# Optimization experiments

Measured on AMD Instinct MI355X. Metric: run time of the kernel, lower is better.

Reference implementation:

```python
import jax, jax.numpy as jnp
import numpy as np

EPS = 1e-5

def wn(v, g):
    # weight_norm dim=0: each output row scaled to norm g
    return v * (g / jnp.linalg.norm(v, axis=1))[:, None]

def layernorm(h):
    mu = jnp.mean(h, axis=-1, keepdims=True)
    var = jnp.mean(jnp.square(h - mu), axis=-1, keepdims=True)
    return (h - mu) / jnp.sqrt(var + EPS)

def setup_inputs() -> dict:
    key = jax.random.key(0)
    ks = jax.random.split(key, 12)
    N, G = 200000, 256
    node_dim, cond_dim, out_dim = 256, 256, 512
    H = out_dim // 2  # 256
    s = lambda d: 1.0 / np.sqrt(d)
    return {
        "x": jax.random.normal(ks[0], (N, node_dim), jnp.float32),
        "cond": jax.random.normal(ks[1], (G, cond_dim), jnp.float32),
        "batch_ids": jax.random.randint(ks[2], (N,), 0, G, jnp.int32),
        # FiLM cond projection: Linear(cond_dim, 2H) weight-normed, with bias
        "v_cond": jax.random.normal(ks[3], (2 * H, cond_dim), jnp.float32) * s(cond_dim),
        "g_cond": jnp.ones((2 * H,), jnp.float32),
        "b_cond": jnp.zeros((2 * H,), jnp.float32),
        # FiLM main linear: Linear(node_dim, H) weight-normed, no bias
        "v1": jax.random.normal(ks[4], (H, node_dim), jnp.float32) * s(node_dim),
        "g1": jnp.ones((H,), jnp.float32),
        # head MLP: Linear(H,H)+ReLU+Linear(H,out_dim), both weight-normed, with bias
        "v2": jax.random.normal(ks[5], (H, H), jnp.float32) * s(H),
        "g2": jnp.ones((H,), jnp.float32),
        "b2": jnp.zeros((H,), jnp.float32),
        "v3": jax.random.normal(ks[6], (out_dim, H), jnp.float32) * s(H),
        "g3": jnp.ones((out_dim,), jnp.float32),
        "b3": jnp.zeros((out_dim,), jnp.float32),
    }

def reference(x, cond, batch_ids, v_cond, g_cond, b_cond, v1, g1, v2, g2, b2, v3, g3, b3):
    H = v1.shape[0]
    # per-graph FiLM params
    gb = cond @ wn(v_cond, g_cond).T + b_cond          # [G, 2H]
    gamma = gb[:, :H] + 1.0                            # [G, H]
    beta = gb[:, H:]                                   # [G, H]
    # node path: linear (no bias) + layernorm (no affine)
    h = layernorm(x @ wn(v1, g1).T)                    # [N, H]
    # gather per-graph FiLM to nodes, modulate, relu
    h = jax.nn.relu(h * gamma[batch_ids] + beta[batch_ids])
    # head MLP
    h = jax.nn.relu(h @ wn(v2, g2).T + b2)             # [N, H]
    logits = h @ wn(v3, g3).T + b3                     # [N, out_dim]
    return logits
```

## Files before the change

kernel.cpp:

```cpp
#include <hip/hip_runtime.h>

typedef __bf16 bf16x8 __attribute__((ext_vector_type(8)));
typedef float f32x16 __attribute__((ext_vector_type(16)));

#define K_DIM 256

__global__ void wn_kernel(const float* __restrict__ v, const float* __restrict__ gv,
                          __bf16* __restrict__ dstb, float* __restrict__ dstf) {
  const int r = blockIdx.x;
  const int l = threadIdx.x;
  const float* vr = v + (size_t)r * K_DIM;
  float4 p = *reinterpret_cast<const float4*>(vr + l * 4);
  float ss = p.x * p.x + p.y * p.y + p.z * p.z + p.w * p.w;
#pragma unroll
  for (int m = 1; m <= 32; m <<= 1) ss += __shfl_xor(ss, m, 64);
  const float sc = gv[r] * rsqrtf(ss);
  const float a0 = p.x * sc, a1 = p.y * sc, a2 = p.z * sc, a3 = p.w * sc;
  if (dstf != nullptr) {
    float4 o; o.x = a0; o.y = a1; o.z = a2; o.w = a3;
    *reinterpret_cast<float4*>(dstf + (size_t)r * K_DIM + l * 4) = o;
  }
  if (dstb != nullptr) {
    const int rows = gridDim.x;
    __bf16* d = dstb + ((size_t)(l >> 1) * rows + r) * 8 + (l & 1) * 4;
    d[0] = (__bf16)a0; d[1] = (__bf16)a1; d[2] = (__bf16)a2; d[3] = (__bf16)a3;
  }
}

__global__ void gb_kernel(const float* __restrict__ cond, const float* __restrict__ wncf,
                          const float* __restrict__ bc, float* __restrict__ gbuf) {
  const int gidx = blockIdx.x;
  const int t = threadIdx.x;
  __shared__ float c[256];
  c[t] = cond[(size_t)gidx * 256 + t];
  __syncthreads();
#pragma unroll
  for (int h = 0; h < 2; ++h) {
    const int o = (h << 8) + t;
    const float* wr = wncf + (size_t)o * 256;
    float s = 0.0f;
#pragma unroll 8
    for (int k = 0; k < 256; k += 4) {
      const float4 w4 = *reinterpret_cast<const float4*>(wr + k);
      s += c[k] * w4.x + c[k + 1] * w4.y + c[k + 2] * w4.z + c[k + 3] * w4.w;
    }
    gbuf[(size_t)gidx * 512 + o] = s + bc[o] + (h == 0 ? 1.0f : 0.0f);
  }
}

__global__ __launch_bounds__(128, 2) void fused_kernel(
    const float* __restrict__ x, const int* __restrict__ bids,
    const __bf16* __restrict__ W1t, const __bf16* __restrict__ W2t,
    const __bf16* __restrict__ W3t, const float* __restrict__ gbuf,
    const float* __restrict__ b2, const float* __restrict__ b3,
    float* __restrict__ out, const int n) {
  __shared__ __bf16 Abuf[32 * 64 * 8];
  __shared__ __bf16 Wbuf[4 * 256 * 8];

  const int t = threadIdx.x;
  const int lane = t & 63;
  const int wave = t >> 6;
  const int nlo = lane & 31;
  const int g = lane >> 5;
  const int mbase = wave << 5;
  const int R = blockIdx.x << 6;

  f32x16 zero;
#pragma unroll
  for (int e = 0; e < 16; ++e) zero[e] = 0.0f;

  f32x16 acc[8];

  auto stage_w = [&](const __bf16* wsrc, int kt, int outr, int outbase) {
#pragma unroll
    for (int it = 0; it < 8; ++it) {
      const int cid = (((wave << 3) + it) << 6) + lane;
      const int kc = cid >> 8;
      const int outl = cid & 255;
      const __bf16* gp = wsrc + ((size_t)((kt * 4 + kc) * outr + outbase + outl) << 3);
      __builtin_amdgcn_global_load_lds(
          (__attribute__((address_space(1))) void*)gp,
          (__attribute__((address_space(3))) void*)(&Wbuf[((wave << 3) + it) << 9]),
          16, 0, 0);
    }
  };

#pragma unroll
  for (int nt = 0; nt < 8; ++nt) acc[nt] = zero;
  {
    int row = R + mbase + nlo;
    if (row >= n) row = n - 1;
    const float* xrow = x + (size_t)row * K_DIM;
    for (int kt = 0; kt < 8; ++kt) {
      __syncthreads();
      stage_w(W1t, kt, 256, 0);
      __syncthreads();
#pragma unroll
      for (int ks = 0; ks < 2; ++ks) {
        const int k0 = kt * 32 + ks * 16 + g * 8;
        const float4 p = *reinterpret_cast<const float4*>(xrow + k0);
        const float4 q = *reinterpret_cast<const float4*>(xrow + k0 + 4);
        bf16x8 a;
        a[0] = (__bf16)p.x; a[1] = (__bf16)p.y; a[2] = (__bf16)p.z; a[3] = (__bf16)p.w;
        a[4] = (__bf16)q.x; a[5] = (__bf16)q.y; a[6] = (__bf16)q.z; a[7] = (__bf16)q.w;
#pragma unroll
        for (int nt = 0; nt < 8; ++nt) {
          const bf16x8 b = *reinterpret_cast<const bf16x8*>(
              &Wbuf[((((ks << 1) + g) << 8) + (nt << 5) + nlo) << 3]);
          acc[nt] = __builtin_amdgcn_mfma_f32_32x32x16_bf16(a, b, acc[nt], 0, 0, 0);
        }
      }
    }
  }

  {
    float mu[16], rs[16];
#pragma unroll
    for (int reg = 0; reg < 16; ++reg) {
      float s = 0.0f, q = 0.0f;
#pragma unroll
      for (int nt = 0; nt < 8; ++nt) {
        const float v = acc[nt][reg];
        s += v; q += v * v;
      }
#pragma unroll
      for (int m = 1; m <= 16; m <<= 1) {
        s += __shfl_xor(s, m, 64);
        q += __shfl_xor(q, m, 64);
      }
      const float mean = s * (1.0f / 256.0f);
      const float var = q * (1.0f / 256.0f) - mean * mean;
      mu[reg] = mean;
      rs[reg] = rsqrtf(var + 1e-5f);
    }
#pragma unroll
    for (int reg = 0; reg < 16; ++reg) {
      const int rl = (reg & 3) + ((reg >> 2) << 3) + (g << 2);
      int rglob = R + mbase + rl;
      if (rglob >= n) rglob = n - 1;
      const int bid = bids[rglob];
      const float* grow = gbuf + ((size_t)bid << 9);
#pragma unroll
      for (int nt = 0; nt < 8; ++nt) {
        const int col = (nt << 5) + nlo;
        float v = (acc[nt][reg] - mu[reg]) * rs[reg];
        v = v * grow[col] + grow[256 + col];
        v = v > 0.0f ? v : 0.0f;
        Abuf[((((col >> 3) << 6) + mbase + rl) << 3) + (col & 7)] = (__bf16)v;
      }
    }
  }

#pragma unroll
  for (int nt = 0; nt < 8; ++nt) acc[nt] = zero;
  for (int kt = 0; kt < 8; ++kt) {
    __syncthreads();
    stage_w(W2t, kt, 256, 0);
    __syncthreads();
#pragma unroll
    for (int ks = 0; ks < 2; ++ks) {
      const int kc = kt * 4 + ks * 2 + g;
      const bf16x8 a = *reinterpret_cast<const bf16x8*>(
          &Abuf[((kc << 6) + mbase + nlo) << 3]);
#pragma unroll
      for (int nt = 0; nt < 8; ++nt) {
        const bf16x8 b = *reinterpret_cast<const bf16x8*>(
            &Wbuf[((((ks << 1) + g) << 8) + (nt << 5) + nlo) << 3]);
        acc[nt] = __builtin_amdgcn_mfma_f32_32x32x16_bf16(a, b, acc[nt], 0, 0, 0);
      }
    }
  }
  {
    float b2v[8];
#pragma unroll
    for (int nt = 0; nt < 8; ++nt) b2v[nt] = b2[(nt << 5) + nlo];
#pragma unroll
    for (int reg = 0; reg < 16; ++reg) {
      const int rl = (reg & 3) + ((reg >> 2) << 3) + (g << 2);
#pragma unroll
      for (int nt = 0; nt < 8; ++nt) {
        const int col = (nt << 5) + nlo;
        float v = acc[nt][reg] + b2v[nt];
        v = v > 0.0f ? v : 0.0f;
        Abuf[((((col >> 3) << 6) + mbase + rl) << 3) + (col & 7)] = (__bf16)v;
      }
    }
  }

  for (int half = 0; half < 2; ++half) {
#pragma unroll
    for (int nt = 0; nt < 8; ++nt) acc[nt] = zero;
    for (int kt = 0; kt < 8; ++kt) {
      __syncthreads();
      stage_w(W3t, kt, 512, half << 8);
      __syncthreads();
#pragma unroll
      for (int ks = 0; ks < 2; ++ks) {
        const int kc = kt * 4 + ks * 2 + g;
        const bf16x8 a = *reinterpret_cast<const bf16x8*>(
            &Abuf[((kc << 6) + mbase + nlo) << 3]);
#pragma unroll
        for (int nt = 0; nt < 8; ++nt) {
          const bf16x8 b = *reinterpret_cast<const bf16x8*>(
              &Wbuf[((((ks << 1) + g) << 8) + (nt << 5) + nlo) << 3]);
          acc[nt] = __builtin_amdgcn_mfma_f32_32x32x16_bf16(a, b, acc[nt], 0, 0, 0);
        }
      }
    }
    float b3v[8];
#pragma unroll
    for (int nt = 0; nt < 8; ++nt) b3v[nt] = b3[(half << 8) + (nt << 5) + nlo];
#pragma unroll
    for (int reg = 0; reg < 16; ++reg) {
      const int rl = (reg & 3) + ((reg >> 2) << 3) + (g << 2);
      const int rglob = R + mbase + rl;
      if (rglob < n) {
        float* orow = out + (size_t)rglob * 512 + (half << 8);
#pragma unroll
        for (int nt = 0; nt < 8; ++nt) orow[(nt << 5) + nlo] = acc[nt][reg] + b3v[nt];
      }
    }
  }
}

extern "C" void kernel_launch(void* const* d_in, const int* in_sizes, int n_in,
                              void* d_out, int out_size, void* d_ws, size_t ws_size,
                              hipStream_t stream) {
  const float* x      = (const float*)d_in[0];
  const float* cond   = (const float*)d_in[1];
  const int*   bids   = (const int*)d_in[2];
  const float* v_cond = (const float*)d_in[3];
  const float* g_cond = (const float*)d_in[4];
  const float* b_cond = (const float*)d_in[5];
  const float* v1     = (const float*)d_in[6];
  const float* g1     = (const float*)d_in[7];
  const float* v2     = (const float*)d_in[8];
  const float* g2     = (const float*)d_in[9];
  const float* b2     = (const float*)d_in[10];
  const float* v3     = (const float*)d_in[11];
  const float* g3     = (const float*)d_in[12];
  const float* b3     = (const float*)d_in[13];
  float* out = (float*)d_out;
  const int n = in_sizes[0] / K_DIM;

  char* ws = (char*)d_ws;
  __bf16* W1t = (__bf16*)ws;
  __bf16* W2t = W1t + 65536;
  __bf16* W3t = W2t + 65536;
  float* wncf = (float*)(W3t + 131072);
  float* gbuf = wncf + 131072;

  wn_kernel<<<256, 64, 0, stream>>>(v1, g1, W1t, nullptr);
  wn_kernel<<<256, 64, 0, stream>>>(v2, g2, W2t, nullptr);
  wn_kernel<<<512, 64, 0, stream>>>(v3, g3, W3t, nullptr);
  wn_kernel<<<512, 64, 0, stream>>>(v_cond, g_cond, nullptr, wncf);
  gb_kernel<<<256, 256, 0, stream>>>(cond, wncf, b_cond, gbuf);

  const int nb = (n + 63) / 64;
  fused_kernel<<<nb, 128, 0, stream>>>(x, bids, W1t, W2t, W3t, gbuf, b2, b3, out, n);
}
```

Before: 722.2 us.

## Split fused MLP across 8 waves with double-buffered weight staging

Measured after the change: 785.7 us. 1.09x slower.

```diff
diff --git a/kernel.cpp b/kernel.cpp
--- a/kernel.cpp
+++ b/kernel.cpp
@@ -48,78 +48,134 @@
   }
 }
 
-__global__ __launch_bounds__(128, 2) void fused_kernel(
+__global__ __launch_bounds__(512, 4) void fused_kernel(
     const float* __restrict__ x, const int* __restrict__ bids,
     const __bf16* __restrict__ W1t, const __bf16* __restrict__ W2t,
     const __bf16* __restrict__ W3t, const float* __restrict__ gbuf,
     const float* __restrict__ b2, const float* __restrict__ b3,
     float* __restrict__ out, const int n) {
   __shared__ __bf16 Abuf[32 * 64 * 8];
-  __shared__ __bf16 Wbuf[4 * 256 * 8];
+  __shared__ __bf16 Wbuf[2][4 * 256 * 8];
 
   const int t = threadIdx.x;
   const int lane = t & 63;
-  const int wave = t >> 6;
+  const int w = t >> 6;
+  const int wrow = w & 1;
+  const int wcol = w >> 1;
   const int nlo = lane & 31;
   const int g = lane >> 5;
-  const int mbase = wave << 5;
+  const int mbase = wrow << 5;
+  const int colbase = wcol << 6;
   const int R = blockIdx.x << 6;
 
   f32x16 zero;
 #pragma unroll
   for (int e = 0; e < 16; ++e) zero[e] = 0.0f;
 
-  f32x16 acc[8];
-
-  auto stage_w = [&](const __bf16* wsrc, int kt, int outr, int outbase) {
-#pragma unroll
-    for (int it = 0; it < 8; ++it) {
-      const int cid = (((wave << 3) + it) << 6) + lane;
+  f32x16 acc[2];
+
+  auto stage_w = [&](int buf, const __bf16* wsrc, int kt, int outr, int outbase) {
+#pragma unroll
+    for (int it = 0; it < 2; ++it) {
+      const int cid = (it << 9) + t;
       const int kc = cid >> 8;
       const int outl = cid & 255;
       const __bf16* gp = wsrc + ((size_t)((kt * 4 + kc) * outr + outbase + outl) << 3);
       __builtin_amdgcn_global_load_lds(
           (__attribute__((address_space(1))) void*)gp,
-          (__attribute__((address_space(3))) void*)(&Wbuf[((wave << 3) + it) << 9]),
+          (__attribute__((address_space(3))) void*)(&Wbuf[buf][((it << 9) + (w << 6)) << 3]),
           16, 0, 0);
     }
   };
 
-#pragma unroll
-  for (int nt = 0; nt < 8; ++nt) acc[nt] = zero;
+  auto pass_lds = [&](const __bf16* wsrc, int outr, int outbase) {
+    stage_w(0, wsrc, 0, outr, outbase);
+    __syncthreads();
+#pragma unroll
+    for (int kt = 0; kt < 8; ++kt) {
+      const int cur = kt & 1;
+      if (kt < 7) stage_w(cur ^ 1, wsrc, kt + 1, outr, outbase);
+#pragma unroll
+      for (int ks = 0; ks < 2; ++ks) {
+        const int kcf = kt * 4 + ks * 2 + g;
+        const bf16x8 a = *reinterpret_cast<const bf16x8*>(
+            &Abuf[((kcf << 6) + mbase + nlo) << 3]);
+#pragma unroll
+        for (int nt = 0; nt < 2; ++nt) {
+          const bf16x8 b = *reinterpret_cast<const bf16x8*>(
+              &Wbuf[cur][((((ks << 1) + g) << 8) + colbase + (nt << 5) + nlo) << 3]);
+          acc[nt] = __builtin_amdgcn_mfma_f32_32x32x16_bf16(a, b, acc[nt], 0, 0, 0);
+        }
+      }
+      __syncthreads();
+    }
+  };
+
+#pragma unroll
+  for (int nt = 0; nt < 2; ++nt) acc[nt] = zero;
   {
     int row = R + mbase + nlo;
     if (row >= n) row = n - 1;
     const float* xrow = x + (size_t)row * K_DIM;
+
+    stage_w(0, W1t, 0, 256, 0);
+    float4 xf[2][4];
+#pragma unroll
+    for (int i = 0; i < 2; ++i) {
+      xf[0][2 * i]     = *reinterpret_cast<const float4*>(xrow + (i << 4) + (g << 3));
+      xf[0][2 * i + 1] = *reinterpret_cast<const float4*>(xrow + (i << 4) + (g << 3) + 4);
+    }
+    __syncthreads();
+
+#pragma unroll
     for (int kt = 0; kt < 8; ++kt) {
+      const int cur = kt & 1;
+      if (kt < 7) stage_w(cur ^ 1, W1t, kt + 1, 256, 0);
+      bf16x8 a[2];
+#pragma unroll
+      for (int ks = 0; ks < 2; ++ks) {
+        const float4 p = xf[cur][2 * ks], q = xf[cur][2 * ks + 1];
+        a[ks][0] = (__bf16)p.x; a[ks][1] = (__bf16)p.y;
+        a[ks][2] = (__bf16)p.z; a[ks][3] = (__bf16)p.w;
+        a[ks][4] = (__bf16)q.x; a[ks][5] = (__bf16)q.y;
+        a[ks][6] = (__bf16)q.z; a[ks][7] = (__bf16)q.w;
+      }
+      if (kt < 7) {
+        const float* xb = xrow + ((kt + 1) << 5) + (g << 3);
+#pragma unroll
+        for (int i = 0; i < 2; ++i) {
+          xf[cur ^ 1][2 * i]     = *reinterpret_cast<const float4*>(xb + (i << 4));
+          xf[cur ^ 1][2 * i + 1] = *reinterpret_cast<const float4*>(xb + (i << 4) + 4);
+        }
+      }
+#pragma unroll
+      for (int ks = 0; ks < 2; ++ks) {
+#pragma unroll
+        for (int nt = 0; nt < 2; ++nt) {
+          const bf16x8 b = *reinterpret_cast<const bf16x8*>(
+              &Wbuf[cur][((((ks << 1) + g) << 8) + colbase + (nt << 5) + nlo) << 3]);
+          acc[nt] = __builtin_amdgcn_mfma_f32_32x32x16_bf16(a[ks], b, acc[nt], 0, 0, 0);
+        }
+      }
       __syncthreads();
-      stage_w(W1t, kt, 256, 0);
-      __syncthreads();
-#pragma unroll
-      for (int ks = 0; ks < 2; ++ks) {
-        const int k0 = kt * 32 + ks * 16 + g * 8;
-        const float4 p = *reinterpret_cast<const float4*>(xrow + k0);
-        const float4 q = *reinterpret_cast<const float4*>(xrow + k0 + 4);
-        bf16x8 a;
-        a[0] = (__bf16)p.x; a[1] = (__bf16)p.y; a[2] = (__bf16)p.z; a[3] = (__bf16)p.w;
-        a[4] = (__bf16)q.x; a[5] = (__bf16)q.y; a[6] = (__bf16)q.z; a[7] = (__bf16)q.w;
-#pragma unroll
-        for (int nt = 0; nt < 8; ++nt) {
-          const bf16x8 b = *reinterpret_cast<const bf16x8*>(
-              &Wbuf[((((ks << 1) + g) << 8) + (nt << 5) + nlo) << 3]);
-          acc[nt] = __builtin_amdgcn_mfma_f32_32x32x16_bf16(a, b, acc[nt], 0, 0, 0);
-        }
-      }
     }
   }
 
   {
-    float mu[16], rs[16];
+    float* red = reinterpret_cast<float*>(&Wbuf[0][0]);
+    int bidv[16];
+#pragma unroll
+    for (int reg = 0; reg < 16; ++reg) {
+      const int rl = (reg & 3) + ((reg >> 2) << 3) + (g << 2);
+      int rglob = R + mbase + rl;
+      if (rglob >= n) rglob = n - 1;
+      bidv[reg] = bids[rglob];
+    }
 #pragma unroll
     for (int reg = 0; reg < 16; ++reg) {
       float s = 0.0f, q = 0.0f;
 #pragma unroll
-      for (int nt = 0; nt < 8; ++nt) {
+      for (int nt = 0; nt < 2; ++nt) {
         const float v = acc[nt][reg];
         s += v; q += v * v;
       }
@@ -128,88 +184,68 @@
         s += __shfl_xor(s, m, 64);
         q += __shfl_xor(q, m, 64);
       }
+      if (nlo == 0) {
+        const int rl = (reg & 3) + ((reg >> 2) << 3) + (g << 2);
+        const int row = mbase + rl;
+        red[(row << 3) + (wcol << 1)] = s;
+        red[(row << 3) + (wcol << 1) + 1] = q;
+      }
+    }
+    __syncthreads();
+#pragma unroll
+    for (int reg = 0; reg < 16; ++reg) {
+      const int rl = (reg & 3) + ((reg >> 2) << 3) + (g << 2);
+      const int row = mbase + rl;
+      const float4 f1 = *reinterpret_cast<const float4*>(&red[row << 3]);
+      const float4 f2 = *reinterpret_cast<const float4*>(&red[(row << 3) + 4]);
+      const float s = f1.x + f1.z + f2.x + f2.z;
+      const float q = f1.y + f1.w + f2.y + f2.w;
       const float mean = s * (1.0f / 256.0f);
       const float var = q * (1.0f / 256.0f) - mean * mean;
-      mu[reg] = mean;
-      rs[reg] = rsqrtf(var + 1e-5f);
-    }
-#pragma unroll
-    for (int reg = 0; reg < 16; ++reg) {
-      const int rl = (reg & 3) + ((reg >> 2) << 3) + (g << 2);
-      int rglob = R + mbase + rl;
-      if (rglob >= n) rglob = n - 1;
-      const int bid = bids[rglob];
-      const float* grow = gbuf + ((size_t)bid << 9);
-#pragma unroll
-      for (int nt = 0; nt < 8; ++nt) {
-        const int col = (nt << 5) + nlo;
-        float v = (acc[nt][reg] - mu[reg]) * rs[reg];
+      const float rs = rsqrtf(var + 1e-5f);
+      const float* grow = gbuf + ((size_t)bidv[reg] << 9);
+#pragma unroll
+      for (int nt = 0; nt < 2; ++nt) {
+        const int col = colbase + (nt << 5) + nlo;
+        float v = (acc[nt][reg] - mean) * rs;
         v = v * grow[col] + grow[256 + col];
         v = v > 0.0f ? v : 0.0f;
-        Abuf[((((col >> 3) << 6) + mbase + rl) << 3) + (col & 7)] = (__bf16)v;
-      }
-    }
-  }
-
-#pragma unroll
-  for (int nt = 0; nt < 8; ++nt) acc[nt] = zero;
-  for (int kt = 0; kt < 8; ++kt) {
-    __syncthreads();
-    stage_w(W2t, kt, 256, 0);
-    __syncthreads();
-#pragma unroll
-    for (int ks = 0; ks < 2; ++ks) {
-      const int kc = kt * 4 + ks * 2 + g;
-      const bf16x8 a = *reinterpret_cast<const bf16x8*>(
-          &Abuf[((kc << 6) + mbase + nlo) << 3]);
-#pragma unroll
-      for (int nt = 0; nt < 8; ++nt) {
-        const bf16x8 b = *reinterpret_cast<const bf16x8*>(
-            &Wbuf[((((ks << 1) + g) << 8) + (nt << 5) + nlo) << 3]);
-        acc[nt] = __builtin_amdgcn_mfma_f32_32x32x16_bf16(a, b, acc[nt], 0, 0, 0);
-      }
-    }
-  }
+        Abuf[((((col >> 3) << 6) + row) << 3) + (col & 7)] = (__bf16)v;
+      }
+    }
+  }
+  __syncthreads();
+
+#pragma unroll
+  for (int nt = 0; nt < 2; ++nt) acc[nt] = zero;
+  pass_lds(W2t, 256, 0);
   {
-    float b2v[8];
-#pragma unroll
-    for (int nt = 0; nt < 8; ++nt) b2v[nt] = b2[(nt << 5) + nlo];
-#pragma unroll
-    for (int reg = 0; reg < 16; ++reg) {
-      const int rl = (reg & 3) + ((reg >> 2) << 3) + (g << 2);
-#pragma unroll
-      for (int nt = 0; nt < 8; ++nt) {
-        const int col = (nt << 5) + nlo;
+    float b2v[2];
+#pragma unroll
+    for (int nt = 0; nt < 2; ++nt) b2v[nt] = b2[colbase + (nt << 5) + nlo];
+#pragma unroll
+    for (int reg = 0; reg < 16; ++reg) {
+      const int rl = (reg & 3) + ((reg >> 2) << 3) + (g << 2);
+      const int row = mbase + rl;
+#pragma unroll
+      for (int nt = 0; nt < 2; ++nt) {
+        const int col = colbase + (nt << 5) + nlo;
         float v = acc[nt][reg] + b2v[nt];
         v = v > 0.0f ? v : 0.0f;
-        Abuf[((((col >> 3) << 6) + mbase + rl) << 3) + (col & 7)] = (__bf16)v;
-      }
-    }
-  }
-
+        Abuf[((((col >> 3) << 6) + row) << 3) + (col & 7)] = (__bf16)v;
+      }
+    }
+  }
+  __syncthreads();
+
+#pragma unroll
   for (int half = 0; half < 2; ++half) {
 #pragma unroll
-    for (int nt = 0; nt < 8; ++nt) acc[nt] = zero;
-    for (int kt = 0; kt < 8; ++kt) {
-      __syncthreads();
-      stage_w(W3t, kt, 512, half << 8);
-      __syncthreads();
-#pragma unroll
-      for (int ks = 0; ks < 2; ++ks) {
-        const int kc = kt * 4 + ks * 2 + g;
-        const bf16x8 a = *reinterpret_cast<const bf16x8*>(
-            &Abuf[((kc << 6) + mbase + nlo) << 3]);
-#pragma unroll
-        for (int nt = 0; nt < 8; ++nt) {
-          const bf16x8 b = *reinterpret_cast<const bf16x8*>(
-              &Wbuf[((((ks << 1) + g) << 8) + (nt << 5) + nlo) << 3]);
-          acc[nt] = __builtin_amdgcn_mfma_f32_32x32x16_bf16(a, b, acc[nt], 0, 0, 0);
-        }
-      }
-    }
-    float b3v[8];
-#pragma unroll
-    for (int nt = 0; nt < 8; ++nt) b3v[nt] = b3[(half << 8) + (nt << 5) + nlo];
+    for (int nt = 0; nt < 2; ++nt) acc[nt] = zero;
+    pass_lds(W3t, 512, half << 8);
+    float b3v[2];
+#pragma unroll
+    for (int nt = 0; nt < 2; ++nt) b3v[nt] = b3[(half << 8) + colbase + (nt << 5) + nlo];
 #pragma unroll
     for (int reg = 0; reg < 16; ++reg) {
       const int rl = (reg & 3) + ((reg >> 2) << 3) + (g << 2);
@@ -217,7 +253,8 @@
       if (rglob < n) {
         float* orow = out + (size_t)rglob * 512 + (half << 8);
 #pragma unroll
-        for (int nt = 0; nt < 8; ++nt) orow[(nt << 5) + nlo] = acc[nt][reg] + b3v[nt];
+        for (int nt = 0; nt < 2; ++nt)
+          orow[colbase + (nt << 5) + nlo] = acc[nt][reg] + b3v[nt];
       }
     }
   }
@@ -257,5 +294,5 @@
   gb_kernel<<<256, 256, 0, stream>>>(cond, wncf, b_cond, gbuf);
 
   const int nb = (n + 63) / 64;
-  fused_kernel<<<nb, 128, 0, stream>>>(x, bids, W1t, W2t, W3t, gbuf, b2, b3, out, n);
-}
+  fused_kernel<<<nb, 512, 0, stream>>>(x, bids, W1t, W2t, W3t, gbuf, b2, b3, out, n);
+}
```

## Stage full weight matrices in LDS, split columns across 4 waves, prefetch next stage

Applied to the files above, without the earlier changes.

Measured after the change: 840.0 us. 1.16x slower.

```diff
diff --git a/kernel.cpp b/kernel.cpp
--- a/kernel.cpp
+++ b/kernel.cpp
@@ -21,8 +21,8 @@
     *reinterpret_cast<float4*>(dstf + (size_t)r * K_DIM + l * 4) = o;
   }
   if (dstb != nullptr) {
-    const int rows = gridDim.x;
-    __bf16* d = dstb + ((size_t)(l >> 1) * rows + r) * 8 + (l & 1) * 4;
+    __bf16* d = dstb + ((size_t)(r >> 8) << 16) +
+                ((size_t)((l >> 1) << 8) + (r & 255)) * 8 + (l & 1) * 4;
     d[0] = (__bf16)a0; d[1] = (__bf16)a1; d[2] = (__bf16)a2; d[3] = (__bf16)a3;
   }
 }
@@ -48,78 +48,92 @@
   }
 }
 
-__global__ __launch_bounds__(128, 2) void fused_kernel(
+__global__ __launch_bounds__(256, 1) void fused_kernel(
     const float* __restrict__ x, const int* __restrict__ bids,
     const __bf16* __restrict__ W1t, const __bf16* __restrict__ W2t,
     const __bf16* __restrict__ W3t, const float* __restrict__ gbuf,
     const float* __restrict__ b2, const float* __restrict__ b3,
     float* __restrict__ out, const int n) {
+  __shared__ __bf16 Wbuf[32 * 256 * 8];
   __shared__ __bf16 Abuf[32 * 64 * 8];
-  __shared__ __bf16 Wbuf[4 * 256 * 8];
 
   const int t = threadIdx.x;
   const int lane = t & 63;
-  const int wave = t >> 6;
+  const int w = t >> 6;
+  const int rowg = w & 1;
+  const int colg = w >> 1;
   const int nlo = lane & 31;
   const int g = lane >> 5;
-  const int mbase = wave << 5;
+  const int rowbase = rowg << 5;
+  const int colbase = colg << 7;
   const int R = blockIdx.x << 6;
 
-  f32x16 zero;
-#pragma unroll
-  for (int e = 0; e < 16; ++e) zero[e] = 0.0f;
-
-  f32x16 acc[8];
-
-  auto stage_w = [&](const __bf16* wsrc, int kt, int outr, int outbase) {
-#pragma unroll
-    for (int it = 0; it < 8; ++it) {
-      const int cid = (((wave << 3) + it) << 6) + lane;
-      const int kc = cid >> 8;
-      const int outl = cid & 255;
-      const __bf16* gp = wsrc + ((size_t)((kt * 4 + kc) * outr + outbase + outl) << 3);
+  float* red = reinterpret_cast<float*>(&Wbuf[65024]);
+
+  auto aidx = [](int kc, int row) { return ((kc << 6) + (row ^ (kc & 7))) << 3; };
+
+  auto stage = [&](const __bf16* src, int U) {
+    for (int u = w; u < U; u += 4) {
       __builtin_amdgcn_global_load_lds(
-          (__attribute__((address_space(1))) void*)gp,
-          (__attribute__((address_space(3))) void*)(&Wbuf[((wave << 3) + it) << 9]),
-          16, 0, 0);
+          (__attribute__((address_space(1))) void*)(src + ((size_t)u << 9) + (lane << 3)),
+          (__attribute__((address_space(3))) void*)(&Wbuf[u << 9]), 16, 0, 0);
     }
   };
 
-#pragma unroll
-  for (int nt = 0; nt < 8; ++nt) acc[nt] = zero;
+  f32x16 acc[4];
+  auto zero_acc = [&]() {
+#pragma unroll
+    for (int nt = 0; nt < 4; ++nt)
+#pragma unroll
+      for (int e = 0; e < 16; ++e) acc[nt][e] = 0.0f;
+  };
+
+  stage(W1t, 128);
+
+  int row = R + rowbase + nlo;
+  if (row >= n) row = n - 1;
+  const float* xrow = x + (size_t)row * K_DIM;
+  float4 xp[32];
+#pragma unroll
+  for (int i = 0; i < 16; ++i) {
+    const int kc = (i << 1) + g;
+    xp[2 * i]     = *reinterpret_cast<const float4*>(xrow + (kc << 3));
+    xp[2 * i + 1] = *reinterpret_cast<const float4*>(xrow + (kc << 3) + 4);
+  }
+  int bidv[16];
+#pragma unroll
+  for (int reg = 0; reg < 16; ++reg) {
+    const int rl = (reg & 3) + ((reg >> 2) << 3) + (g << 2);
+    int rg = R + rowbase + rl;
+    if (rg >= n) rg = n - 1;
+    bidv[reg] = bids[rg];
+  }
+  __syncthreads();
+
+  zero_acc();
+#pragma unroll
+  for (int ks = 0; ks < 16; ++ks) {
+    const int kc = (ks << 1) + g;
+    const float4 p = xp[2 * ks], q = xp[2 * ks + 1];
+    bf16x8 a;
+    a[0] = (__bf16)p.x; a[1] = (__bf16)p.y; a[2] = (__bf16)p.z; a[3] = (__bf16)p.w;
+    a[4] = (__bf16)q.x; a[5] = (__bf16)q.y; a[6] = (__bf16)q.z; a[7] = (__bf16)q.w;
+#pragma unroll
+    for (int nt = 0; nt < 4; ++nt) {
+      const bf16x8 b = *reinterpret_cast<const bf16x8*>(
+          &Wbuf[((kc << 8) + colbase + (nt << 5) + nlo) << 3]);
+      acc[nt] = __builtin_amdgcn_mfma_f32_32x32x16_bf16(a, b, acc[nt], 0, 0, 0);
+    }
+  }
+  __syncthreads();
+  stage(W2t, 127);
+
   {
-    int row = R + mbase + nlo;
-    if (row >= n) row = n - 1;
-    const float* xrow = x + (size_t)row * K_DIM;
-    for (int kt = 0; kt < 8; ++kt) {
-      __syncthreads();
-      stage_w(W1t, kt, 256, 0);
-      __syncthreads();
-#pragma unroll
-      for (int ks = 0; ks < 2; ++ks) {
-        const int k0 = kt * 32 + ks * 16 + g * 8;
-        const float4 p = *reinterpret_cast<const float4*>(xrow + k0);
-        const float4 q = *reinterpret_cast<const float4*>(xrow + k0 + 4);
-        bf16x8 a;
-        a[0] = (__bf16)p.x; a[1] = (__bf16)p.y; a[2] = (__bf16)p.z; a[3] = (__bf16)p.w;
-        a[4] = (__bf16)q.x; a[5] = (__bf16)q.y; a[6] = (__bf16)q.z; a[7] = (__bf16)q.w;
-#pragma unroll
-        for (int nt = 0; nt < 8; ++nt) {
-          const bf16x8 b = *reinterpret_cast<const bf16x8*>(
-              &Wbuf[((((ks << 1) + g) << 8) + (nt << 5) + nlo) << 3]);
-          acc[nt] = __builtin_amdgcn_mfma_f32_32x32x16_bf16(a, b, acc[nt], 0, 0, 0);
-        }
-      }
-    }
-  }
-
-  {
-    float mu[16], rs[16];
 #pragma unroll
     for (int reg = 0; reg < 16; ++reg) {
       float s = 0.0f, q = 0.0f;
 #pragma unroll
-      for (int nt = 0; nt < 8; ++nt) {
+      for (int nt = 0; nt < 4; ++nt) {
         const float v = acc[nt][reg];
         s += v; q += v * v;
       }
@@ -128,96 +142,132 @@
         s += __shfl_xor(s, m, 64);
         q += __shfl_xor(q, m, 64);
       }
+      if (nlo == 0) {
+        const int rl = (reg & 3) + ((reg >> 2) << 3) + (g << 2);
+        const int rowi = rowbase + rl;
+        float2 sq; sq.x = s; sq.y = q;
+        *reinterpret_cast<float2*>(&red[(rowi << 2) + (colg << 1)]) = sq;
+      }
+    }
+    __syncthreads();
+#pragma unroll
+    for (int reg = 0; reg < 16; ++reg) {
+      const int rl = (reg & 3) + ((reg >> 2) << 3) + (g << 2);
+      const int rowi = rowbase + rl;
+      const float4 r4 = *reinterpret_cast<const float4*>(&red[rowi << 2]);
+      const float s = r4.x + r4.z, q = r4.y + r4.w;
       const float mean = s * (1.0f / 256.0f);
       const float var = q * (1.0f / 256.0f) - mean * mean;
-      mu[reg] = mean;
-      rs[reg] = rsqrtf(var + 1e-5f);
-    }
-#pragma unroll
-    for (int reg = 0; reg < 16; ++reg) {
-      const int rl = (reg & 3) + ((reg >> 2) << 3) + (g << 2);
-      int rglob = R + mbase + rl;
-      if (rglob >= n) rglob = n - 1;
-      const int bid = bids[rglob];
-      const float* grow = gbuf + ((size_t)bid << 9);
-#pragma unroll
-      for (int nt = 0; nt < 8; ++nt) {
-        const int col = (nt << 5) + nlo;
-        float v = (acc[nt][reg] - mu[reg]) * rs[reg];
+      const float rsv = rsqrtf(var + 1e-5f);
+      const float* grow = gbuf + ((size_t)bidv[reg] << 9);
+#pragma unroll
+      for (int nt = 0; nt < 4; ++nt) {
+        const int col = colbase + (nt << 5) + nlo;
+        float v = (acc[nt][reg] - mean) * rsv;
         v = v * grow[col] + grow[256 + col];
         v = v > 0.0f ? v : 0.0f;
-        Abuf[((((col >> 3) << 6) + mbase + rl) << 3) + (col & 7)] = (__bf16)v;
-      }
-    }
-  }
-
-#pragma unroll
-  for (int nt = 0; nt < 8; ++nt) acc[nt] = zero;
-  for (int kt = 0; kt < 8; ++kt) {
-    __syncthreads();
-    stage_w(W2t, kt, 256, 0);
-    __syncthreads();
-#pragma unroll
-    for (int ks = 0; ks < 2; ++ks) {
-      const int kc = kt * 4 + ks * 2 + g;
-      const bf16x8 a = *reinterpret_cast<const bf16x8*>(
-          &Abuf[((kc << 6) + mbase + nlo) << 3]);
-#pragma unroll
-      for (int nt = 0; nt < 8; ++nt) {
-        const bf16x8 b = *reinterpret_cast<const bf16x8*>(
-            &Wbuf[((((ks << 1) + g) << 8) + (nt << 5) + nlo) << 3]);
-        acc[nt] = __builtin_amdgcn_mfma_f32_32x32x16_bf16(a, b, acc[nt], 0, 0, 0);
-      }
-    }
-  }
+        Abuf[aidx(col >> 3, rowi) + (col & 7)] = (__bf16)v;
+      }
+    }
+  }
+  __syncthreads();
+  if (w == 3) {
+    __builtin_amdgcn_global_load_lds(
+        (__attribute__((address_space(1))) void*)(W2t + ((size_t)127 << 9) + (lane << 3)),
+        (__attribute__((address_space(3))) void*)(&Wbuf[127 << 9]), 16, 0, 0);
+  }
+  __syncthreads();
+
+  zero_acc();
+#pragma unroll
+  for (int ks = 0; ks < 16; ++ks) {
+    const int kc = (ks << 1) + g;
+    const bf16x8 a = *reinterpret_cast<const bf16x8*>(&Abuf[aidx(kc, rowbase + nlo)]);
+#pragma unroll
+    for (int nt = 0; nt < 4; ++nt) {
+      const bf16x8 b = *reinterpret_cast<const bf16x8*>(
+          &Wbuf[((kc << 8) + colbase + (nt << 5) + nlo) << 3]);
+      acc[nt] = __builtin_amdgcn_mfma_f32_32x32x16_bf16(a, b, acc[nt], 0, 0, 0);
+    }
+  }
+  __syncthreads();
+  stage(W3t, 128);
   {
-    float b2v[8];
-#pragma unroll
-    for (int nt = 0; nt < 8; ++nt) b2v[nt] = b2[(nt << 5) + nlo];
+    float b2v[4];
+#pragma unroll
+    for (int nt = 0; nt < 4; ++nt) b2v[nt] = b2[colbase + (nt << 5) + nlo];
 #pragma unroll
     for (int reg = 0; reg < 16; ++reg) {
       const int rl = (reg & 3) + ((reg >> 2) << 3) + (g << 2);
-#pragma unroll
-      for (int nt = 0; nt < 8; ++nt) {
-        const int col = (nt << 5) + nlo;
+      const int rowi = rowbase + rl;
+#pragma unroll
+      for (int nt = 0; nt < 4; ++nt) {
+        const int col = colbase + (nt << 5) + nlo;
         float v = acc[nt][reg] + b2v[nt];
         v = v > 0.0f ? v : 0.0f;
-        Abuf[((((col >> 3) << 6) + mbase + rl) << 3) + (col & 7)] = (__bf16)v;
-      }
-    }
-  }
-
-  for (int half = 0; half < 2; ++half) {
-#pragma unroll
-    for (int nt = 0; nt < 8; ++nt) acc[nt] = zero;
-    for (int kt = 0; kt < 8; ++kt) {
-      __syncthreads();
-      stage_w(W3t, kt, 512, half << 8);
-      __syncthreads();
-#pragma unroll
-      for (int ks = 0; ks < 2; ++ks) {
-        const int kc = kt * 4 + ks * 2 + g;
-        const bf16x8 a = *reinterpret_cast<const bf16x8*>(
-            &Abuf[((kc << 6) + mbase + nlo) << 3]);
-#pragma unroll
-        for (int nt = 0; nt < 8; ++nt) {
-          const bf16x8 b = *reinterpret_cast<const bf16x8*>(
-              &Wbuf[((((ks << 1) + g) << 8) + (nt << 5) + nlo) << 3]);
-          acc[nt] = __builtin_amdgcn_mfma_f32_32x32x16_bf16(a, b, acc[nt], 0, 0, 0);
-        }
-      }
-    }
-    float b3v[8];
-#pragma unroll
-    for (int nt = 0; nt < 8; ++nt) b3v[nt] = b3[(half << 8) + (nt << 5) + nlo];
+        Abuf[aidx(col >> 3, rowi) + (col & 7)] = (__bf16)v;
+      }
+    }
+  }
+  __syncthreads();
+
+  zero_acc();
+#pragma unroll
+  for (int ks = 0; ks < 16; ++ks) {
+    const int kc = (ks << 1) + g;
+    const bf16x8 a = *reinterpret_cast<const bf16x8*>(&Abuf[aidx(kc, rowbase + nlo)]);
+#pragma unroll
+    for (int nt = 0; nt < 4; ++nt) {
+      const bf16x8 b = *reinterpret_cast<const bf16x8*>(
+          &Wbuf[((kc << 8) + colbase + (nt << 5) + nlo) << 3]);
+      acc[nt] = __builtin_amdgcn_mfma_f32_32x32x16_bf16(a, b, acc[nt], 0, 0, 0);
+    }
+  }
+  __syncthreads();
+  stage(W3t + 65536, 128);
+  {
+    float b3v[4];
+#pragma unroll
+    for (int nt = 0; nt < 4; ++nt) b3v[nt] = b3[colbase + (nt << 5) + nlo];
 #pragma unroll
     for (int reg = 0; reg < 16; ++reg) {
       const int rl = (reg & 3) + ((reg >> 2) << 3) + (g << 2);
-      const int rglob = R + mbase + rl;
+      const int rglob = R + rowbase + rl;
       if (rglob < n) {
-        float* orow = out + (size_t)rglob * 512 + (half << 8);
-#pragma unroll
-        for (int nt = 0; nt < 8; ++nt) orow[(nt << 5) + nlo] = acc[nt][reg] + b3v[nt];
+        float* orow = out + (size_t)rglob * 512;
+#pragma unroll
+        for (int nt = 0; nt < 4; ++nt)
+          orow[colbase + (nt << 5) + nlo] = acc[nt][reg] + b3v[nt];
+      }
+    }
+  }
+  __syncthreads();
+
+  zero_acc();
+#pragma unroll
+  for (int ks = 0; ks < 16; ++ks) {
+    const int kc = (ks << 1) + g;
+    const bf16x8 a = *reinterpret_cast<const bf16x8*>(&Abuf[aidx(kc, rowbase + nlo)]);
+#pragma unroll
+    for (int nt = 0; nt < 4; ++nt) {
+      const bf16x8 b = *reinterpret_cast<const bf16x8*>(
+          &Wbuf[((kc << 8) + colbase + (nt << 5) + nlo) << 3]);
+      acc[nt] = __builtin_amdgcn_mfma_f32_32x32x16_bf16(a, b, acc[nt], 0, 0, 0);
+    }
+  }
+  {
+    float b3v[4];
+#pragma unroll
+    for (int nt = 0; nt < 4; ++nt) b3v[nt] = b3[256 + colbase + (nt << 5) + nlo];
+#pragma unroll
+    for (int reg = 0; reg < 16; ++reg) {
+      const int rl = (reg & 3) + ((reg >> 2) << 3) + (g << 2);
+      const int rglob = R + rowbase + rl;
+      if (rglob < n) {
+        float* orow = out + (size_t)rglob * 512 + 256;
+#pragma unroll
+        for (int nt = 0; nt < 4; ++nt)
+          orow[colbase + (nt << 5) + nlo] = acc[nt][reg] + b3v[nt];
       }
     }
   }
@@ -257,5 +307,5 @@
   gb_kernel<<<256, 256, 0, stream>>>(cond, wncf, b_cond, gbuf);
 
   const int nb = (n + 63) / 64;
-  fused_kernel<<<nb, 128, 0, stream>>>(x, bids, W1t, W2t, W3t, gbuf, b2, b3, out, n);
+  fused_kernel<<<nb, 256, 0, stream>>>(x, bids, W1t, W2t, W3t, gbuf, b2, b3, out, n);
 }
```

## Triple-buffer weight tiles with async LDS loads and prefetch node inputs into registers

Applied to the files above, without the earlier changes.

Result: slower. 935.4 us (+29.5%).

```diff
diff --git a/kernel.cpp b/kernel.cpp
--- a/kernel.cpp
+++ b/kernel.cpp
@@ -21,8 +21,8 @@
     *reinterpret_cast<float4*>(dstf + (size_t)r * K_DIM + l * 4) = o;
   }
   if (dstb != nullptr) {
-    const int rows = gridDim.x;
-    __bf16* d = dstb + ((size_t)(l >> 1) * rows + r) * 8 + (l & 1) * 4;
+    __bf16* d = dstb + ((size_t)(r >> 8) << 16) +
+                ((size_t)((l >> 1) << 8) + (r & 255)) * 8 + (l & 1) * 4;
     d[0] = (__bf16)a0; d[1] = (__bf16)a1; d[2] = (__bf16)a2; d[3] = (__bf16)a3;
   }
 }
@@ -48,69 +48,117 @@
   }
 }
 
-__global__ __launch_bounds__(128, 2) void fused_kernel(
+__global__ __launch_bounds__(128, 1) void fused_kernel(
     const float* __restrict__ x, const int* __restrict__ bids,
     const __bf16* __restrict__ W1t, const __bf16* __restrict__ W2t,
     const __bf16* __restrict__ W3t, const float* __restrict__ gbuf,
     const float* __restrict__ b2, const float* __restrict__ b3,
     float* __restrict__ out, const int n) {
   __shared__ __bf16 Abuf[32 * 64 * 8];
-  __shared__ __bf16 Wbuf[4 * 256 * 8];
+  __shared__ __bf16 Wring[3][8192];
 
   const int t = threadIdx.x;
   const int lane = t & 63;
-  const int wave = t >> 6;
+  const int w = t >> 6;
   const int nlo = lane & 31;
   const int g = lane >> 5;
-  const int mbase = wave << 5;
+  const int mbase = w << 5;
   const int R = blockIdx.x << 6;
 
-  f32x16 zero;
-#pragma unroll
-  for (int e = 0; e < 16; ++e) zero[e] = 0.0f;
+  auto aidx = [](int kc, int row) { return ((kc << 6) + (row ^ (kc & 7))) << 3; };
+
+  auto src_of = [&](int tt) -> const __bf16* {
+    const __bf16* p = W1t + ((size_t)tt << 13);
+    if (tt >= 8)  p = W2t + ((size_t)(tt - 8) << 13);
+    if (tt >= 16) p = W3t + ((size_t)(tt - 16) << 13);
+    return p;
+  };
+
+  auto stage = [&](__bf16* dst, const __bf16* src) {
+#pragma unroll
+    for (int i = 0; i < 8; ++i) {
+      const int c = (w << 3) + i;
+      __builtin_amdgcn_global_load_lds(
+          (const __attribute__((address_space(1))) void*)(src + (c << 9) + (lane << 3)),
+          (__attribute__((address_space(3))) void*)(dst + (c << 9)), 16, 0, 0);
+    }
+  };
 
   f32x16 acc[8];
-
-  auto stage_w = [&](const __bf16* wsrc, int kt, int outr, int outbase) {
-#pragma unroll
-    for (int it = 0; it < 8; ++it) {
-      const int cid = (((wave << 3) + it) << 6) + lane;
-      const int kc = cid >> 8;
-      const int outl = cid & 255;
-      const __bf16* gp = wsrc + ((size_t)((kt * 4 + kc) * outr + outbase + outl) << 3);
-      __builtin_amdgcn_global_load_lds(
-          (__attribute__((address_space(1))) void*)gp,
-          (__attribute__((address_space(3))) void*)(&Wbuf[((wave << 3) + it) << 9]),
-          16, 0, 0);
-    }
+  auto zero_acc = [&]() {
+#pragma unroll
+    for (int nt = 0; nt < 8; ++nt)
+#pragma unroll
+      for (int e = 0; e < 16; ++e) acc[nt][e] = 0.0f;
   };
 
-#pragma unroll
-  for (int nt = 0; nt < 8; ++nt) acc[nt] = zero;
-  {
-    int row = R + mbase + nlo;
-    if (row >= n) row = n - 1;
-    const float* xrow = x + (size_t)row * K_DIM;
-    for (int kt = 0; kt < 8; ++kt) {
-      __syncthreads();
-      stage_w(W1t, kt, 256, 0);
-      __syncthreads();
-#pragma unroll
-      for (int ks = 0; ks < 2; ++ks) {
-        const int k0 = kt * 32 + ks * 16 + g * 8;
-        const float4 p = *reinterpret_cast<const float4*>(xrow + k0);
-        const float4 q = *reinterpret_cast<const float4*>(xrow + k0 + 4);
-        bf16x8 a;
-        a[0] = (__bf16)p.x; a[1] = (__bf16)p.y; a[2] = (__bf16)p.z; a[3] = (__bf16)p.w;
-        a[4] = (__bf16)q.x; a[5] = (__bf16)q.y; a[6] = (__bf16)q.z; a[7] = (__bf16)q.w;
-#pragma unroll
-        for (int nt = 0; nt < 8; ++nt) {
-          const bf16x8 b = *reinterpret_cast<const bf16x8*>(
-              &Wbuf[((((ks << 1) + g) << 8) + (nt << 5) + nlo) << 3]);
-          acc[nt] = __builtin_amdgcn_mfma_f32_32x32x16_bf16(a, b, acc[nt], 0, 0, 0);
-        }
-      }
-    }
+  int row = R + mbase + nlo;
+  if (row >= n) row = n - 1;
+  const float* xrow = x + (size_t)row * K_DIM;
+  float4 xp[32];
+#pragma unroll
+  for (int i = 0; i < 16; ++i) {
+    const int kc = (i << 1) + g;
+    xp[2 * i]     = *reinterpret_cast<const float4*>(xrow + (kc << 3));
+    xp[2 * i + 1] = *reinterpret_cast<const float4*>(xrow + (kc << 3) + 4);
+  }
+  int bidv[16];
+#pragma unroll
+  for (int reg = 0; reg < 16; ++reg) {
+    const int rl = (reg & 3) + ((reg >> 2) << 3) + (g << 2);
+    int rg = R + mbase + rl;
+    if (rg >= n) rg = n - 1;
+    bidv[reg] = bids[rg];
+  }
+  float b2v[8], b3v0[8], b3v1[8];
+#pragma unroll
+  for (int nt = 0; nt < 8; ++nt) {
+    const int col = (nt << 5) + nlo;
+    b2v[nt]  = b2[col];
+    b3v0[nt] = b3[col];
+    b3v1[nt] = b3[256 + col];
+  }
+#pragma unroll
+  for (int i = 0; i < 32; ++i)
+    asm volatile("" :: "v"(xp[i].x), "v"(xp[i].y), "v"(xp[i].z), "v"(xp[i].w));
+#pragma unroll
+  for (int reg = 0; reg < 16; ++reg) asm volatile("" :: "v"(bidv[reg]));
+#pragma unroll
+  for (int nt = 0; nt < 8; ++nt)
+    asm volatile("" :: "v"(b2v[nt]), "v"(b3v0[nt]), "v"(b3v1[nt]));
+
+  stage(&Wring[0][0], src_of(0));
+  stage(&Wring[1][0], src_of(1));
+  __bf16* wa = &Wring[0][0];
+  __bf16* wb = &Wring[1][0];
+  __bf16* wc = &Wring[2][0];
+
+#define PIPE_HEAD(TCUR)                                          \
+  asm volatile("s_waitcnt vmcnt(8)" ::: "memory");               \
+  asm volatile("s_barrier" ::: "memory");                        \
+  if ((TCUR) + 2 < 32) stage(wc, src_of((TCUR) + 2));
+
+#define ROTATE() { __bf16* _tmp = wa; wa = wb; wb = wc; wc = _tmp; }
+
+  zero_acc();
+#pragma unroll
+  for (int kt = 0; kt < 8; ++kt) {
+    PIPE_HEAD(kt)
+#pragma unroll
+    for (int ks = 0; ks < 2; ++ks) {
+      const int i = kt * 2 + ks;
+      const float4 p = xp[2 * i], q = xp[2 * i + 1];
+      bf16x8 a;
+      a[0] = (__bf16)p.x; a[1] = (__bf16)p.y; a[2] = (__bf16)p.z; a[3] = (__bf16)p.w;
+      a[4] = (__bf16)q.x; a[5] = (__bf16)q.y; a[6] = (__bf16)q.z; a[7] = (__bf16)q.w;
+#pragma unroll
+      for (int nt = 0; nt < 8; ++nt) {
+        const bf16x8 b = *reinterpret_cast<const bf16x8*>(
+            &wa[((((ks << 1) + g) << 8) + (nt << 5) + nlo) << 3]);
+        acc[nt] = __builtin_amdgcn_mfma_f32_32x32x16_bf16(a, b, acc[nt], 0, 0, 0);
+      }
+    }
+    ROTATE()
   }
 
   {
@@ -136,91 +184,118 @@
 #pragma unroll
     for (int reg = 0; reg < 16; ++reg) {
       const int rl = (reg & 3) + ((reg >> 2) << 3) + (g << 2);
-      int rglob = R + mbase + rl;
-      if (rglob >= n) rglob = n - 1;
-      const int bid = bids[rglob];
-      const float* grow = gbuf + ((size_t)bid << 9);
+      const int rowi = mbase + rl;
+      const float* grow = gbuf + ((size_t)bidv[reg] << 9);
 #pragma unroll
       for (int nt = 0; nt < 8; ++nt) {
         const int col = (nt << 5) + nlo;
         float v = (acc[nt][reg] - mu[reg]) * rs[reg];
         v = v * grow[col] + grow[256 + col];
         v = v > 0.0f ? v : 0.0f;
-        Abuf[((((col >> 3) << 6) + mbase + rl) << 3) + (col & 7)] = (__bf16)v;
-      }
-    }
-  }
-
-#pragma unroll
-  for (int nt = 0; nt < 8; ++nt) acc[nt] = zero;
+        Abuf[aidx(col >> 3, rowi) + (col & 7)] = (__bf16)v;
+      }
+    }
+  }
+
+  zero_acc();
+#pragma unroll
   for (int kt = 0; kt < 8; ++kt) {
-    __syncthreads();
-    stage_w(W2t, kt, 256, 0);
-    __syncthreads();
+    PIPE_HEAD(8 + kt)
 #pragma unroll
     for (int ks = 0; ks < 2; ++ks) {
-      const int kc = kt * 4 + ks * 2 + g;
-      const bf16x8 a = *reinterpret_cast<const bf16x8*>(
-          &Abuf[((kc << 6) + mbase + nlo) << 3]);
+      const int kcf = kt * 4 + ks * 2 + g;
+      const bf16x8 a = *reinterpret_cast<const bf16x8*>(&Abuf[aidx(kcf, mbase + nlo)]);
 #pragma unroll
       for (int nt = 0; nt < 8; ++nt) {
         const bf16x8 b = *reinterpret_cast<const bf16x8*>(
-            &Wbuf[((((ks << 1) + g) << 8) + (nt << 5) + nlo) << 3]);
+            &wa[((((ks << 1) + g) << 8) + (nt << 5) + nlo) << 3]);
         acc[nt] = __builtin_amdgcn_mfma_f32_32x32x16_bf16(a, b, acc[nt], 0, 0, 0);
       }
     }
+    ROTATE()
   }
   {
-    float b2v[8];
-#pragma unroll
-    for (int nt = 0; nt < 8; ++nt) b2v[nt] = b2[(nt << 5) + nlo];
 #pragma unroll
     for (int reg = 0; reg < 16; ++reg) {
       const int rl = (reg & 3) + ((reg >> 2) << 3) + (g << 2);
+      const int rowi = mbase + rl;
 #pragma unroll
       for (int nt = 0; nt < 8; ++nt) {
         const int col = (nt << 5) + nlo;
         float v = acc[nt][reg] + b2v[nt];
         v = v > 0.0f ? v : 0.0f;
-        Abuf[((((col >> 3) << 6) + mbase + rl) << 3) + (col & 7)] = (__bf16)v;
-      }
-    }
-  }
-
-  for (int half = 0; half < 2; ++half) {
-#pragma unroll
-    for (int nt = 0; nt < 8; ++nt) acc[nt] = zero;
-    for (int kt = 0; kt < 8; ++kt) {
-      __syncthreads();
-      stage_w(W3t, kt, 512, half << 8);
-      __syncthreads();
-#pragma unroll
-      for (int ks = 0; ks < 2; ++ks) {
-        const int kc = kt * 4 + ks * 2 + g;
-        const bf16x8 a = *reinterpret_cast<const bf16x8*>(
-            &Abuf[((kc << 6) + mbase + nlo) << 3]);
-#pragma unroll
-        for (int nt = 0; nt < 8; ++nt) {
-          const bf16x8 b = *reinterpret_cast<const bf16x8*>(
-              &Wbuf[((((ks << 1) + g) << 8) + (nt << 5) + nlo) << 3]);
-          acc[nt] = __builtin_amdgcn_mfma_f32_32x32x16_bf16(a, b, acc[nt], 0, 0, 0);
-        }
-      }
-    }
-    float b3v[8];
-#pragma unroll
-    for (int nt = 0; nt < 8; ++nt) b3v[nt] = b3[(half << 8) + (nt << 5) + nlo];
+        Abuf[aidx(col >> 3, rowi) + (col & 7)] = (__bf16)v;
+      }
+    }
+  }
+
+  zero_acc();
+#pragma unroll
+  for (int kt = 0; kt < 8; ++kt) {
+    PIPE_HEAD(16 + kt)
+#pragma unroll
+    for (int ks = 0; ks < 2; ++ks) {
+      const int kcf = kt * 4 + ks * 2 + g;
+      const bf16x8 a = *reinterpret_cast<const bf16x8*>(&Abuf[aidx(kcf, mbase + nlo)]);
+#pragma unroll
+      for (int nt = 0; nt < 8; ++nt) {
+        const bf16x8 b = *reinterpret_cast<const bf16x8*>(
+            &wa[((((ks << 1) + g) << 8) + (nt << 5) + nlo) << 3]);
+        acc[nt] = __builtin_amdgcn_mfma_f32_32x32x16_bf16(a, b, acc[nt], 0, 0, 0);
+      }
+    }
+    ROTATE()
+  }
+  {
 #pragma unroll
     for (int reg = 0; reg < 16; ++reg) {
       const int rl = (reg & 3) + ((reg >> 2) << 3) + (g << 2);
       const int rglob = R + mbase + rl;
       if (rglob < n) {
-        float* orow = out + (size_t)rglob * 512 + (half << 8);
-#pragma unroll
-        for (int nt = 0; nt < 8; ++nt) orow[(nt << 5) + nlo] = acc[nt][reg] + b3v[nt];
-      }
-    }
-  }
+        float* orow = out + (size_t)rglob * 512;
+#pragma unroll
+        for (int nt = 0; nt < 8; ++nt) orow[(nt << 5) + nlo] = acc[nt][reg] + b3v0[nt];
+      }
+    }
+  }
+
+  zero_acc();
+#pragma unroll
+  for (int kt = 0; kt < 8; ++kt) {
+    if (kt == 7) {
+      asm volatile("s_waitcnt vmcnt(0)" ::: "memory");
+    } else {
+      asm volatile("s_waitcnt vmcnt(8)" ::: "memory");
+    }
+    asm volatile("s_barrier" ::: "memory");
+    if (24 + kt + 2 < 32) stage(wc, src_of(24 + kt + 2));
+#pragma unroll
+    for (int ks = 0; ks < 2; ++ks) {
+      const int kcf = kt * 4 + ks * 2 + g;
+      const bf16x8 a = *reinterpret_cast<const bf16x8*>(&Abuf[aidx(kcf, mbase + nlo)]);
+#pragma unroll
+      for (int nt = 0; nt < 8; ++nt) {
+        const bf16x8 b = *reinterpret_cast<const bf16x8*>(
+            &wa[((((ks << 1) + g) << 8) + (nt << 5) + nlo) << 3]);
+        acc[nt] = __builtin_amdgcn_mfma_f32_32x32x16_bf16(a, b, acc[nt], 0, 0, 0);
+      }
+    }
+    ROTATE()
+  }
+  {
+#pragma unroll
+    for (int reg = 0; reg < 16; ++reg) {
+      const int rl = (reg & 3) + ((reg >> 2) << 3) + (g << 2);
+      const int rglob = R + mbase + rl;
+      if (rglob < n) {
+        float* orow = out + (size_t)rglob * 512 + 256;
+#pragma unroll
+        for (int nt = 0; nt < 8; ++nt) orow[(nt << 5) + nlo] = acc[nt][reg] + b3v1[nt];
+      }
+    }
+  }
+#undef PIPE_HEAD
+#undef ROTATE
 }
 
 extern "C" void kernel_launch(void* const* d_in, const int* in_sizes, int n_in,
```
